# Performance work log

Hardware: AMD Instinct MI355X
Metric: run time of the kernel (lower is better)

Reference implementation:

```python
import jax, jax.numpy as jnp
import numpy as np
import math

N, T, V, C = 64, 256, 25, 64  # batch, frames, joints, channels (in==out)
D = C  # out_channels
EPS = 1e-5


def _shift_indices(v, c):
    i = np.arange(v)[:, None]
    j = np.arange(c)[None, :]
    shift_in = ((i * c + j + j * c) % (c * v)).reshape(-1)
    shift_out = ((i * c + j - j * c) % (c * v)).reshape(-1)
    return shift_in.astype(np.int64), shift_out.astype(np.int64)


def setup_inputs() -> dict:
    key = jax.random.key(0)
    k1, k2 = jax.random.split(key)
    si, so = _shift_indices(V, D)
    return {
        "x0": jax.random.normal(k1, (N, T, V, C), dtype=jnp.float32),
        "Linear_weight": jax.random.normal(k2, (C, D), dtype=jnp.float32) * math.sqrt(1.0 / D),
        "Linear_bias": jnp.zeros((1, 1, D), dtype=jnp.float32),
        "Feature_Mask": jnp.zeros((1, V, C), dtype=jnp.float32),
        "gamma": jnp.ones((V * D,), dtype=jnp.float32),
        "beta": jnp.zeros((V * D,), dtype=jnp.float32),
        "shift_in": jnp.asarray(si),
        "shift_out": jnp.asarray(so),
    }


def reference(x0, Linear_weight, Linear_bias, Feature_Mask, gamma, beta, shift_in, shift_out):
    n, t, v, c = x0.shape
    d = Linear_weight.shape[1]
    # shift-in gather over flattened (node, channel) axis
    x = x0.reshape(n * t, v * c)[:, shift_in].reshape(n * t, v, c)
    # learned feature mask (tanh + 1)
    x = x * (jnp.tanh(Feature_Mask) + 1.0)
    # pointwise channel transform + bias
    x = jnp.einsum('nwc,cd->nwd', x, Linear_weight) + Linear_bias
    # shift-out gather
    x = x.reshape(n * t, v * d)[:, shift_out]
    # BatchNorm1d (training mode): batch stats over n*t rows, biased var
    mean = jnp.mean(x, axis=0)
    var = jnp.var(x, axis=0)
    x = (x - mean) * (gamma / jnp.sqrt(var + EPS)) + beta
    # residual (in_channels == out_channels -> identity down) + ReLU
    y = jax.nn.relu(x.reshape(n, t, v, d) + x0)
    # original returns (n, out_channels, t, v)
    return jnp.transpose(y, (0, 3, 1, 2))
```

## Files before the change

kernel.cpp:

```cpp
#include <hip/hip_runtime.h>
#include <math.h>


#define LDW 68

__global__ void k_prep(const float* __restrict__ mask, float* __restrict__ ws) {
  int i = blockIdx.x * 256 + threadIdx.x;
  if (i < 1600) {
    int w = i >> 6, c = i & 63;
    int wr = (w + c) % 25;
    ws[wr * 64 + c] = tanhf(mask[i]) + 1.0f;
  }
  if (i < 3200) ws[1600 + i] = 0.0f;
}

__global__ void k_finalize(const float* __restrict__ gamma,
                           const float* __restrict__ beta,
                           float* __restrict__ ws) {
  int q = blockIdx.x * 256 + threadIdx.x;
  if (q >= 1600) return;
  const float inv = 1.0f / 16384.0f;
  float mean = ws[1600 + q] * inv;
  float var  = ws[3200 + q] * inv - mean * mean;
  float istd = rsqrtf(var + 1e-5f);
  int w = q >> 6, d = q & 63;
  int wp = (w + d) % 25;
  int p  = wp * 64 + d;
  float mul = gamma[p] * istd;
  ws[4800 + q] = mul;
  ws[6400 + q] = beta[p] - mean * mul;
}

template<int PASS>
__launch_bounds__(256, 4)
__global__ void k_main(const float* __restrict__ x0,
                       const float* __restrict__ Wg,
                       float* ws,
                       float* __restrict__ out) {
  __shared__ float s_W[4096];
  __shared__ float s_maskr[1600];
  __shared__ float s_xy[2][1904];

  const int tid = threadIdx.x;

  for (int i = tid; i < 4096; i += 256) s_W[i] = Wg[i];
  for (int i = tid; i < 1600; i += 256) s_maskr[i] = ws[i];

  const bool active = tid < 224;
  const int rs = tid / 112;
  const int rr = tid % 112;
  const int d0 = (rr % 16) * 4;
  const int w0 = (rr / 16) * 4;

  float cmul[16], cadd[16];
  if constexpr (PASS == 2) {
    if (active) {
      #pragma unroll
      for (int i = 0; i < 4; ++i)
        #pragma unroll
        for (int j = 0; j < 4; ++j) {
          int q = (w0 + i) * 64 + d0 + j;
          cmul[i * 4 + j] = ws[4800 + q];
          cadd[i * 4 + j] = ws[6400 + q];
        }
    }
  }

  float ssum[16], ssq[16];
  if constexpr (PASS == 1) {
    #pragma unroll
    for (int k = 0; k < 16; ++k) { ssum[k] = 0.f; ssq[k] = 0.f; }
  }

  const int row_base = blockIdx.x * 16;
  const int n  = row_base >> 8;
  const int t0 = row_base & 255;

  __syncthreads();

  for (int rp = 0; rp < 16; rp += 2) {
    const float* xrow = x0 + (size_t)(row_base + rp) * 1600;

    for (int i4 = tid; i4 < 800; i4 += 256) {
      float4 v = ((const float4*)xrow)[i4];
      int r2 = (i4 >= 400) ? 1 : 0;
      int p4 = (i4 - r2 * 400) * 4;
      float4 m = *(const float4*)&s_maskr[p4];
      int wr = p4 >> 6;
      int c  = p4 & 63;
      float va[4] = {v.x, v.y, v.z, v.w};
      float ma[4] = {m.x, m.y, m.z, m.w};
      int base = wr + 75 - c;
      #pragma unroll
      for (int j = 0; j < 4; ++j) {
        int w = (base - j) % 25;
        s_xy[r2][w * LDW + c + j] = va[j] * ma[j];
      }
    }
    __syncthreads();

    float acc[4][4];
    if (active) {
      #pragma unroll
      for (int i = 0; i < 4; ++i)
        #pragma unroll
        for (int j = 0; j < 4; ++j) acc[i][j] = 0.f;
      for (int c = 0; c < 64; c += 4) {
        float A[4][4], B[4][4];
        #pragma unroll
        for (int i = 0; i < 4; ++i)
          *(float4*)A[i] = *(const float4*)&s_xy[rs][(w0 + i) * LDW + c];
        #pragma unroll
        for (int k = 0; k < 4; ++k)
          *(float4*)B[k] = *(const float4*)&s_W[(c + k) * 64 + d0];
        #pragma unroll
        for (int i = 0; i < 4; ++i)
          #pragma unroll
          for (int j = 0; j < 4; ++j)
            #pragma unroll
            for (int k = 0; k < 4; ++k)
              acc[i][j] = fmaf(A[i][k], B[k][j], acc[i][j]);
      }
    }

    if constexpr (PASS == 1) {
      if (active) {
        #pragma unroll
        for (int i = 0; i < 4; ++i) {
          if (w0 + i < 25) {
            #pragma unroll
            for (int j = 0; j < 4; ++j) {
              ssum[i * 4 + j] += acc[i][j];
              ssq [i * 4 + j]  = fmaf(acc[i][j], acc[i][j], ssq[i * 4 + j]);
            }
          }
        }
      }
      __syncthreads();
    } else {
      __syncthreads();
      if (active) {
        const float* xres = xrow + rs * 1600;
        #pragma unroll
        for (int i = 0; i < 4; ++i) {
          int w = w0 + i;
          if (w < 25) {
            #pragma unroll
            for (int j = 0; j < 4; ++j) {
              int d = d0 + j;
              int k = i * 4 + j;
              int wp = (w + d) % 25;
              float vv = fmaf(acc[i][j], cmul[k], cadd[k]) + xres[wp * 64 + d];
              s_xy[rs][d * 28 + wp] = fmaxf(vv, 0.f);
            }
          }
        }
      }
      __syncthreads();
      for (int i = tid; i < 3200; i += 256) {
        int d   = i / 50;
        int rem = i - d * 50;
        int r2  = rem / 25;
        int wp  = rem - r2 * 25;
        int t   = t0 + rp + r2;
        out[(size_t)(((n * 64 + d) * 256 + t) * 25 + wp)] = s_xy[r2][d * 28 + wp];
      }
      __syncthreads();
    }
  }

  if constexpr (PASS == 1) {
    float* comb = &s_xy[0][0];
    for (int i = tid; i < 3200; i += 256) comb[i] = 0.f;
    __syncthreads();
    if (active) {
      #pragma unroll
      for (int i = 0; i < 4; ++i) {
        int w = w0 + i;
        if (w < 25) {
          #pragma unroll
          for (int j = 0; j < 4; ++j) {
            int q = w * 64 + d0 + j;
            atomicAdd(&comb[q],        ssum[i * 4 + j]);
            atomicAdd(&comb[1600 + q], ssq [i * 4 + j]);
          }
        }
      }
    }
    __syncthreads();
    for (int i = tid; i < 3200; i += 256) {
      atomicAdd(&ws[1600 + i], comb[i]);
    }
  }
}

extern "C" void kernel_launch(void* const* d_in, const int* in_sizes, int n_in,
                              void* d_out, int out_size, void* d_ws, size_t ws_size,
                              hipStream_t stream) {
  const float* x0    = (const float*)d_in[0];
  const float* W     = (const float*)d_in[1];
  const float* mask  = (const float*)d_in[3];
  const float* gamma = (const float*)d_in[4];
  const float* beta  = (const float*)d_in[5];
  float* ws  = (float*)d_ws;
  float* out = (float*)d_out;

  k_prep    <<<13,   256, 0, stream>>>(mask, ws);
  k_main<1> <<<1024, 256, 0, stream>>>(x0, W, ws, out);
  k_finalize<<<7,    256, 0, stream>>>(gamma, beta, ws);
  k_main<2> <<<1024, 256, 0, stream>>>(x0, W, ws, out);
}
```

Before: 407.6 us.

## Use bf16 MFMA for channel GEMM with swizzled LDS and staged residual

Replaces the scalar FP32 FMA GEMM with bf16 MFMA 16x16x32 instructions. Weights are held as register fragments, and activations are staged in an XOR-swizzled bf16 LDS tile padded to 32 rows per frame. The mask is stored as bf16. Pass 2 also keeps the raw x0 rows in LDS so the residual add reads shared memory instead of global. This cuts compute-issue cost and global re-reads, but adds bf16 rounding error to both the batch statistics and the output.

```diff
diff --git a/kernel.cpp b/kernel.cpp
--- a/kernel.cpp
+++ b/kernel.cpp
@@ -2,14 +2,24 @@
 #include <math.h>
 
 
-#define LDW 68
+typedef __attribute__((ext_vector_type(8))) short bf16x8;
+typedef __attribute__((ext_vector_type(4))) float f32x4;
+
+__device__ __forceinline__ ushort f2bf(float f) {
+  uint u; __builtin_memcpy(&u, &f, 4);
+  u += 0x7fffu + ((u >> 16) & 1u);
+  return (ushort)(u >> 16);
+}
+__device__ __forceinline__ float bf2f(ushort b) {
+  uint u = ((uint)b) << 16; float f; __builtin_memcpy(&f, &u, 4); return f;
+}
 
 __global__ void k_prep(const float* __restrict__ mask, float* __restrict__ ws) {
   int i = blockIdx.x * 256 + threadIdx.x;
   if (i < 1600) {
     int w = i >> 6, c = i & 63;
     int wr = (w + c) % 25;
-    ws[wr * 64 + c] = tanhf(mask[i]) + 1.0f;
+    ((ushort*)ws)[wr * 64 + c] = f2bf(tanhf(mask[i]) + 1.0f);
   }
   if (i < 3200) ws[1600 + i] = 0.0f;
 }
@@ -24,8 +34,7 @@
   float var  = ws[3200 + q] * inv - mean * mean;
   float istd = rsqrtf(var + 1e-5f);
   int w = q >> 6, d = q & 63;
-  int wp = (w + d) % 25;
-  int p  = wp * 64 + d;
+  int p = ((w + d) % 25) * 64 + d;
   float mul = gamma[p] * istd;
   ws[4800 + q] = mul;
   ws[6400 + q] = beta[p] - mean * mul;
@@ -37,45 +46,57 @@
                        const float* __restrict__ Wg,
                        float* ws,
                        float* __restrict__ out) {
-  __shared__ float s_W[4096];
-  __shared__ float s_maskr[1600];
-  __shared__ float s_xy[2][1904];
+  __shared__ __align__(8)  ushort s_maskm[1600];
+  __shared__ __align__(16) ushort s_A[4096];
+  __shared__ float s_raw[PASS == 2 ? 3400 : 4];
+  __shared__ float s_aux[3200];
 
   const int tid = threadIdx.x;
-
-  for (int i = tid; i < 4096; i += 256) s_W[i] = Wg[i];
-  for (int i = tid; i < 1600; i += 256) s_maskr[i] = ws[i];
-
-  const bool active = tid < 224;
-  const int rs = tid / 112;
-  const int rr = tid % 112;
-  const int d0 = (rr % 16) * 4;
-  const int w0 = (rr / 16) * 4;
+  const int lr  = tid & 63;
+  const int wid = tid >> 6;
+
+  for (int i = tid; i < 800; i += 256)
+    ((uint*)s_maskm)[i] = ((const uint*)ws)[i];
+  for (int i = tid; i < 2048; i += 256)
+    ((uint*)s_A)[i] = 0u;
+
+  bf16x8 wfrag[2][4];
+  #pragma unroll
+  for (int ks = 0; ks < 2; ++ks)
+    #pragma unroll
+    for (int nt = 0; nt < 4; ++nt) {
+      const int d = nt * 16 + (lr & 15);
+      const int cb = ks * 32 + (lr >> 4) * 8;
+      #pragma unroll
+      for (int j = 0; j < 8; ++j)
+        wfrag[ks][nt][j] = (short)f2bf(Wg[(cb + j) * 64 + d]);
+    }
 
   float cmul[16], cadd[16];
+  float ssum[16], ssq[16];
+  #pragma unroll
+  for (int k = 0; k < 16; ++k) { ssum[k] = 0.f; ssq[k] = 0.f; }
   if constexpr (PASS == 2) {
-    if (active) {
-      #pragma unroll
-      for (int i = 0; i < 4; ++i)
-        #pragma unroll
-        for (int j = 0; j < 4; ++j) {
-          int q = (w0 + i) * 64 + d0 + j;
-          cmul[i * 4 + j] = ws[4800 + q];
-          cadd[i * 4 + j] = ws[6400 + q];
-        }
-    }
-  }
-
-  float ssum[16], ssq[16];
-  if constexpr (PASS == 1) {
-    #pragma unroll
-    for (int k = 0; k < 16; ++k) { ssum[k] = 0.f; ssq[k] = 0.f; }
+    #pragma unroll
+    for (int nt = 0; nt < 4; ++nt)
+      #pragma unroll
+      for (int r = 0; r < 4; ++r) {
+        int row = wid * 16 + (lr >> 4) * 4 + r;
+        int w = row & 31;
+        int d = nt * 16 + (lr & 15);
+        int qq = (w < 25) ? (w * 64 + d) : 0;
+        cmul[nt * 4 + r] = ws[4800 + qq];
+        cadd[nt * 4 + r] = ws[6400 + qq];
+      }
   }
 
   const int row_base = blockIdx.x * 16;
   const int n  = row_base >> 8;
   const int t0 = row_base & 255;
 
+  if constexpr (PASS == 1) {
+    for (int i = tid; i < 3200; i += 256) s_aux[i] = 0.f;
+  }
   __syncthreads();
 
   for (int rp = 0; rp < 16; rp += 2) {
@@ -85,112 +106,95 @@
       float4 v = ((const float4*)xrow)[i4];
       int r2 = (i4 >= 400) ? 1 : 0;
       int p4 = (i4 - r2 * 400) * 4;
-      float4 m = *(const float4*)&s_maskr[p4];
-      int wr = p4 >> 6;
-      int c  = p4 & 63;
+      int wr = p4 >> 6, c0 = p4 & 63;
+      if constexpr (PASS == 2)
+        *(float4*)&s_raw[r2 * 1700 + wr * 68 + c0] = v;
+      uint2 mm = *(const uint2*)&s_maskm[p4];
       float va[4] = {v.x, v.y, v.z, v.w};
-      float ma[4] = {m.x, m.y, m.z, m.w};
-      int base = wr + 75 - c;
+      float ma[4] = {bf2f((ushort)(mm.x & 0xffff)), bf2f((ushort)(mm.x >> 16)),
+                     bf2f((ushort)(mm.y & 0xffff)), bf2f((ushort)(mm.y >> 16))};
+      int wbase = wr + 100 - c0;
       #pragma unroll
       for (int j = 0; j < 4; ++j) {
-        int w = (base - j) % 25;
-        s_xy[r2][w * LDW + c + j] = va[j] * ma[j];
+        int w = (wbase - j) % 25;
+        int row = r2 * 32 + w;
+        int byte = (row * 128 + (c0 + j) * 2) ^ ((w & 7) << 4);
+        *(ushort*)((char*)s_A + byte) = f2bf(va[j] * ma[j]);
       }
     }
     __syncthreads();
 
-    float acc[4][4];
-    if (active) {
-      #pragma unroll
-      for (int i = 0; i < 4; ++i)
+    const int arow = wid * 16 + (lr & 15);
+    bf16x8 afrag[2];
+    #pragma unroll
+    for (int ks = 0; ks < 2; ++ks) {
+      int byte = (arow * 128 + ks * 64 + (lr >> 4) * 16) ^ ((arow & 7) << 4);
+      afrag[ks] = *(const bf16x8*)((const char*)s_A + byte);
+    }
+    f32x4 acc[4];
+    #pragma unroll
+    for (int nt = 0; nt < 4; ++nt) {
+      acc[nt] = (f32x4){0.f, 0.f, 0.f, 0.f};
+      #pragma unroll
+      for (int ks = 0; ks < 2; ++ks)
+        acc[nt] = __builtin_amdgcn_mfma_f32_16x16x32_bf16(afrag[ks], wfrag[ks][nt], acc[nt], 0, 0, 0);
+    }
+
+    if constexpr (PASS == 1) {
+      #pragma unroll
+      for (int nt = 0; nt < 4; ++nt)
         #pragma unroll
-        for (int j = 0; j < 4; ++j) acc[i][j] = 0.f;
-      for (int c = 0; c < 64; c += 4) {
-        float A[4][4], B[4][4];
+        for (int r = 0; r < 4; ++r) {
+          float y = acc[nt][r];
+          ssum[nt * 4 + r] += y;
+          ssq [nt * 4 + r]  = fmaf(y, y, ssq[nt * 4 + r]);
+        }
+      __syncthreads();
+    } else {
+      #pragma unroll
+      for (int nt = 0; nt < 4; ++nt)
         #pragma unroll
-        for (int i = 0; i < 4; ++i)
-          *(float4*)A[i] = *(const float4*)&s_xy[rs][(w0 + i) * LDW + c];
-        #pragma unroll
-        for (int k = 0; k < 4; ++k)
-          *(float4*)B[k] = *(const float4*)&s_W[(c + k) * 64 + d0];
-        #pragma unroll
-        for (int i = 0; i < 4; ++i)
-          #pragma unroll
-          for (int j = 0; j < 4; ++j)
-            #pragma unroll
-            for (int k = 0; k < 4; ++k)
-              acc[i][j] = fmaf(A[i][k], B[k][j], acc[i][j]);
-      }
-    }
-
-    if constexpr (PASS == 1) {
-      if (active) {
-        #pragma unroll
-        for (int i = 0; i < 4; ++i) {
-          if (w0 + i < 25) {
-            #pragma unroll
-            for (int j = 0; j < 4; ++j) {
-              ssum[i * 4 + j] += acc[i][j];
-              ssq [i * 4 + j]  = fmaf(acc[i][j], acc[i][j], ssq[i * 4 + j]);
-            }
+        for (int r = 0; r < 4; ++r) {
+          int row = wid * 16 + (lr >> 4) * 4 + r;
+          int r2 = row >> 5;
+          int w  = row & 31;
+          if (w < 25) {
+            int d  = nt * 16 + (lr & 15);
+            int wp = (w + d) % 25;
+            float y = fmaf(acc[nt][r], cmul[nt * 4 + r], cadd[nt * 4 + r]);
+            y += s_raw[r2 * 1700 + wp * 68 + d];
+            s_aux[d * 50 + r2 * 25 + wp] = fmaxf(y, 0.f);
           }
         }
-      }
       __syncthreads();
-    } else {
-      __syncthreads();
-      if (active) {
-        const float* xres = xrow + rs * 1600;
-        #pragma unroll
-        for (int i = 0; i < 4; ++i) {
-          int w = w0 + i;
-          if (w < 25) {
-            #pragma unroll
-            for (int j = 0; j < 4; ++j) {
-              int d = d0 + j;
-              int k = i * 4 + j;
-              int wp = (w + d) % 25;
-              float vv = fmaf(acc[i][j], cmul[k], cadd[k]) + xres[wp * 64 + d];
-              s_xy[rs][d * 28 + wp] = fmaxf(vv, 0.f);
-            }
-          }
-        }
-      }
-      __syncthreads();
+      const size_t obase = (size_t)n * 409600 + (size_t)(t0 + rp) * 25;
       for (int i = tid; i < 3200; i += 256) {
         int d   = i / 50;
         int rem = i - d * 50;
         int r2  = rem / 25;
         int wp  = rem - r2 * 25;
-        int t   = t0 + rp + r2;
-        out[(size_t)(((n * 64 + d) * 256 + t) * 25 + wp)] = s_xy[r2][d * 28 + wp];
+        out[obase + (size_t)d * 6400 + r2 * 25 + wp] = s_aux[i];
       }
       __syncthreads();
     }
   }
 
   if constexpr (PASS == 1) {
-    float* comb = &s_xy[0][0];
-    for (int i = tid; i < 3200; i += 256) comb[i] = 0.f;
+    #pragma unroll
+    for (int nt = 0; nt < 4; ++nt)
+      #pragma unroll
+      for (int r = 0; r < 4; ++r) {
+        int row = wid * 16 + (lr >> 4) * 4 + r;
+        int w = row & 31;
+        if (w < 25) {
+          int q = w * 64 + nt * 16 + (lr & 15);
+          atomicAdd(&s_aux[q],        ssum[nt * 4 + r]);
+          atomicAdd(&s_aux[1600 + q], ssq [nt * 4 + r]);
+        }
+      }
     __syncthreads();
-    if (active) {
-      #pragma unroll
-      for (int i = 0; i < 4; ++i) {
-        int w = w0 + i;
-        if (w < 25) {
-          #pragma unroll
-          for (int j = 0; j < 4; ++j) {
-            int q = w * 64 + d0 + j;
-            atomicAdd(&comb[q],        ssum[i * 4 + j]);
-            atomicAdd(&comb[1600 + q], ssq [i * 4 + j]);
-          }
-        }
-      }
-    }
-    __syncthreads();
-    for (int i = tid; i < 3200; i += 256) {
-      atomicAdd(&ws[1600 + i], comb[i]);
-    }
+    for (int i = tid; i < 3200; i += 256)
+      atomicAdd(&ws[1600 + i], s_aux[i]);
   }
 }
 
```

New measurement: 346.7 us. 1.18x faster.
